# Performance work log

Hardware: AMD Instinct MI355X
Metric: run time of the kernel (lower is better)

Reference implementation:

```python
import jax, jax.numpy as jnp
import numpy as np

NUM_EXPERTS = 8
TOP_K = 2
HIDDEN = 1024
INTER = 1408
B, S = 2, 1024


def setup_inputs() -> dict:
    key = jax.random.key(0)
    k1, k2, k3, k4, k5 = jax.random.split(key, 5)
    scale = 0.02  # keep activations well-scaled
    return {
        "hidden_states": jax.random.normal(k1, (B, S, HIDDEN), dtype=jnp.float32),
        "gate_w": jax.random.normal(k2, (HIDDEN, NUM_EXPERTS), dtype=jnp.float32) * scale,
        "w_gate": jax.random.normal(k3, (NUM_EXPERTS, HIDDEN, INTER), dtype=jnp.float32) * scale,
        "w_up": jax.random.normal(k4, (NUM_EXPERTS, HIDDEN, INTER), dtype=jnp.float32) * scale,
        "w_down": jax.random.normal(k5, (NUM_EXPERTS, INTER, HIDDEN), dtype=jnp.float32) * scale,
    }


def reference(hidden_states, gate_w, w_gate, w_up, w_down):
    b, s, h = hidden_states.shape
    x = hidden_states.reshape(-1, h)  # [T, H]
    # Router: softmax in fp32, top-k, renormalize over selected experts
    logits = x @ gate_w  # [T, E]
    probs = jax.nn.softmax(logits.astype(jnp.float32), axis=-1)
    rw, sel = jax.lax.top_k(probs, TOP_K)  # [T, K]
    rw = rw / jnp.sum(rw, axis=-1, keepdims=True)
    rw = rw.astype(x.dtype)
    # Per-(token, expert) combine weight; duplicates summed (matches torch mask sum)
    combine = jnp.sum(rw[:, :, None] * jax.nn.one_hot(sel, NUM_EXPERTS, dtype=x.dtype), axis=1)  # [T, E]
    out = jnp.zeros_like(x)
    for e in range(NUM_EXPERTS):  # fixed small structural loop over experts
        inter = jax.nn.silu(x @ w_gate[e]) * (x @ w_up[e])  # [T, I]
        out = out + (inter @ w_down[e]) * combine[:, e:e + 1]
    return out.reshape(b, s, h)
```

## Files before the change

### kernel.cpp

```cpp
#include <hip/hip_runtime.h>
#include <hip/hip_bf16.h>

#define T_TOKENS 2048
#define HID 1024
#define ISZ 1408
#define NEXP 8
#define TILES_MAX 72

typedef __bf16 bf16x8 __attribute__((ext_vector_type(8)));
typedef __bf16 bf16x4 __attribute__((ext_vector_type(4)));
typedef float  f32x16 __attribute__((ext_vector_type(16)));

__device__ __forceinline__ void gload16(const void* g, void* l) {
    __builtin_amdgcn_global_load_lds(
        (const __attribute__((address_space(1))) void*)g,
        (__attribute__((address_space(3))) void*)l,
        16, 0, 0);
}

#define PIPE_BARRIER(N)                                              \
    asm volatile("s_waitcnt vmcnt(" #N ") lgkmcnt(0)" ::: "memory"); \
    __builtin_amdgcn_sched_barrier(0);                               \
    __builtin_amdgcn_s_barrier();                                    \
    __builtin_amdgcn_sched_barrier(0);

__global__ __launch_bounds__(256) void prep_kernel(
    const float* __restrict__ x, const float* __restrict__ gw,
    int* __restrict__ sel, float* __restrict__ wt, __bf16* __restrict__ xb,
    const float* __restrict__ wg, const float* __restrict__ wu,
    __bf16* __restrict__ wgT, __bf16* __restrict__ wuT)
{
    __shared__ __bf16 tb[2][64][70];
    const int bid = blockIdx.x;
    const int tid = threadIdx.x;

    if (bid < 512) {
        const int wave = tid >> 6;
        const int lane = tid & 63;
        const int t = bid * 4 + wave;
        const float* xr = x + (size_t)t * HID;

        const int c0 = lane * 16;
        float4 v0 = *(const float4*)(xr + c0);
        float4 v1 = *(const float4*)(xr + c0 + 4);
        float4 v2 = *(const float4*)(xr + c0 + 8);
        float4 v3 = *(const float4*)(xr + c0 + 12);
        {
            bf16x8 o0, o1;
            o0[0]=(__bf16)v0.x; o0[1]=(__bf16)v0.y; o0[2]=(__bf16)v0.z; o0[3]=(__bf16)v0.w;
            o0[4]=(__bf16)v1.x; o0[5]=(__bf16)v1.y; o0[6]=(__bf16)v1.z; o0[7]=(__bf16)v1.w;
            o1[0]=(__bf16)v2.x; o1[1]=(__bf16)v2.y; o1[2]=(__bf16)v2.z; o1[3]=(__bf16)v2.w;
            o1[4]=(__bf16)v3.x; o1[5]=(__bf16)v3.y; o1[6]=(__bf16)v3.z; o1[7]=(__bf16)v3.w;
            *(bf16x8*)(xb + (size_t)t * HID + c0) = o0;
            *(bf16x8*)(xb + (size_t)t * HID + c0 + 8) = o1;
        }
        if (bid == 0 && tid < 128) {
            bf16x8 z8;
            #pragma unroll
            for (int j = 0; j < 8; ++j) z8[j] = (__bf16)0.f;
            *(bf16x8*)(xb + (size_t)T_TOKENS * HID + tid * 8) = z8;
        }

        float le[8] = {0.f, 0.f, 0.f, 0.f, 0.f, 0.f, 0.f, 0.f};
        float xv[16];
        xv[0]=v0.x; xv[1]=v0.y; xv[2]=v0.z; xv[3]=v0.w;
        xv[4]=v1.x; xv[5]=v1.y; xv[6]=v1.z; xv[7]=v1.w;
        xv[8]=v2.x; xv[9]=v2.y; xv[10]=v2.z; xv[11]=v2.w;
        xv[12]=v3.x; xv[13]=v3.y; xv[14]=v3.z; xv[15]=v3.w;
        #pragma unroll
        for (int j = 0; j < 16; ++j) {
            const float* gr = gw + (size_t)(c0 + j) * NEXP;
            float4 g0 = *(const float4*)gr;
            float4 g1 = *(const float4*)(gr + 4);
            le[0] += xv[j] * g0.x; le[1] += xv[j] * g0.y;
            le[2] += xv[j] * g0.z; le[3] += xv[j] * g0.w;
            le[4] += xv[j] * g1.x; le[5] += xv[j] * g1.y;
            le[6] += xv[j] * g1.z; le[7] += xv[j] * g1.w;
        }
        #pragma unroll
        for (int d = 1; d < 64; d <<= 1) {
            #pragma unroll
            for (int k = 0; k < 8; ++k) le[k] += __shfl_xor(le[k], d);
        }
        float m = le[0];
        #pragma unroll
        for (int k = 1; k < 8; ++k) m = fmaxf(m, le[k]);
        float pe[8]; float s = 0.f;
        #pragma unroll
        for (int k = 0; k < 8; ++k) { pe[k] = expf(le[k] - m); s += pe[k]; }
        int e1 = 0; float p1 = pe[0];
        #pragma unroll
        for (int k = 1; k < 8; ++k) if (pe[k] > p1) { p1 = pe[k]; e1 = k; }
        int e2 = -1; float p2 = -1.f;
        #pragma unroll
        for (int k = 0; k < 8; ++k) if (k != e1 && pe[k] > p2) { p2 = pe[k]; e2 = k; }
        if (lane == 0) {
            float inv = 1.0f / (p1 + p2);
            sel[t * 2 + 0] = e1; sel[t * 2 + 1] = e2;
            wt[t * 2 + 0] = p1 * inv; wt[t * 2 + 1] = p2 * inv;
        }
        return;
    }

    const int f   = bid - 512;
    const int z   = f / 176;
    const int rem = f % 176;
    const int bx  = rem / 16;
    const int by  = rem & 15;
    const int e   = z & 7;
    const int R = HID, C = ISZ;
    const float* in = (z < 8 ? wg : wu) + (size_t)e * R * C;
    __bf16* out = (z < 8 ? wgT : wuT) + (size_t)e * R * C;
    const int rrA = by * 64, rrB = rrA;
    const int ccA = bx * 128, ccB = ccA + 64;
    const int lr  = tid >> 4;
    const int lc4 = (tid & 15) * 4;

    auto loadcvt = [&](int buf, int rr, int cc) {
        #pragma unroll
        for (int p = 0; p < 4; ++p) {
            float4 v = *(const float4*)(in + (size_t)(rr + p * 16 + lr) * C + cc + lc4);
            bf16x4 w;
            w[0] = (__bf16)v.x; w[1] = (__bf16)v.y; w[2] = (__bf16)v.z; w[3] = (__bf16)v.w;
            *(bf16x4*)&tb[buf][p * 16 + lr][lc4] = w;
        }
    };
    auto storeT = [&](int buf, int rr, int cc) {
        #pragma unroll
        for (int q = 0; q < 2; ++q) {
            const int oc = (tid >> 3) + 32 * q;
            const int vs = (tid & 7) * 8;
            bf16x8 w;
            #pragma unroll
            for (int j = 0; j < 8; ++j) w[j] = tb[buf][vs + j][oc];
            *(bf16x8*)(out + (size_t)(cc + oc) * R + rr + vs) = w;
        }
    };

    loadcvt(0, rrA, ccA);
    __syncthreads();
    loadcvt(1, rrB, ccB);
    storeT(0, rrA, ccA);
    __syncthreads();
    storeT(1, rrB, ccB);
}

__global__ __launch_bounds__(1024) void scan_assign_kernel(
    int* __restrict__ tiles,
    const int* __restrict__ sel, const float* __restrict__ wt,
    int* __restrict__ rtok, float* __restrict__ rwt, int* __restrict__ tok2row)
{
    __shared__ int hist[NEXP];
    __shared__ int soff[NEXP];
    __shared__ int scur[NEXP];
    if (threadIdx.x < NEXP) { hist[threadIdx.x] = 0; scur[threadIdx.x] = 0; }
    __syncthreads();
    for (int t = threadIdx.x; t < T_TOKENS; t += 1024) {
        atomicAdd(&hist[sel[t * 2 + 0]], 1);
        atomicAdd(&hist[sel[t * 2 + 1]], 1);
    }
    __syncthreads();
    if (threadIdx.x == 0) {
        int cur = 0, tix = 0;
        for (int e = 0; e < NEXP; ++e) {
            soff[e] = cur;
            int n64 = (hist[e] + 63) & ~63;
            for (int rt = 0; rt * 64 < n64; ++rt)
                tiles[tix++] = (e << 16) | (cur + rt * 64);
            cur += n64;
        }
        for (; tix < TILES_MAX; ++tix) tiles[tix] = -1;
    }
    __syncthreads();
    for (int t = threadIdx.x; t < T_TOKENS; t += 1024) {
        #pragma unroll
        for (int k = 0; k < 2; ++k) {
            int e = sel[t * 2 + k];
            int pos = atomicAdd(&scur[e], 1);
            int row = soff[e] + pos;
            rtok[row] = t + 1;
            rwt[row] = wt[t * 2 + k];
            tok2row[t * 2 + k] = row;
        }
    }
}

__global__ __launch_bounds__(256) void ffn1_kernel(
    const __bf16* __restrict__ xb, const int* __restrict__ rtok,
    const __bf16* __restrict__ wgT, const __bf16* __restrict__ wuT,
    const int* __restrict__ tiles, __bf16* __restrict__ inter,
    const float* __restrict__ wd, __bf16* __restrict__ wdT)
{
    __shared__ __align__(16) char smem[36864];
    const int n   = blockIdx.x;
    const int tid = threadIdx.x;

    if (n >= 22 * TILES_MAX) {
        auto tb = (__bf16 (*)[64][70])smem;
        const int f   = n - 22 * TILES_MAX;
        const int e   = f / 176;
        const int rem = f % 176;
        const int bx  = rem / 16;
        const int by  = rem & 15;
        const int R = ISZ, C = HID;
        const float* in = wd + (size_t)e * R * C;
        __bf16* out = wdT + (size_t)e * R * C;
        const int ccA = by * 64, ccB = ccA;
        const int rrA = bx * 128, rrB = rrA + 64;
        const int lr  = tid >> 4;
        const int lc4 = (tid & 15) * 4;

        auto loadcvt = [&](int buf, int rr, int cc) {
            #pragma unroll
            for (int p = 0; p < 4; ++p) {
                float4 v = *(const float4*)(in + (size_t)(rr + p * 16 + lr) * C + cc + lc4);
                bf16x4 w;
                w[0] = (__bf16)v.x; w[1] = (__bf16)v.y; w[2] = (__bf16)v.z; w[3] = (__bf16)v.w;
                *(bf16x4*)&tb[buf][p * 16 + lr][lc4] = w;
            }
        };
        auto storeT = [&](int buf, int rr, int cc) {
            #pragma unroll
            for (int q = 0; q < 2; ++q) {
                const int oc = (tid >> 3) + 32 * q;
                const int vs = (tid & 7) * 8;
                bf16x8 w;
                #pragma unroll
                for (int j = 0; j < 8; ++j) w[j] = tb[buf][vs + j][oc];
                *(bf16x8*)(out + (size_t)(cc + oc) * R + rr + vs) = w;
            }
        };

        loadcvt(0, rrA, ccA);
        __syncthreads();
        loadcvt(1, rrB, ccB);
        storeT(0, rrA, ccA);
        __syncthreads();
        storeT(1, rrB, ccB);
        return;
    }

    auto sA = (__bf16 (*)[64][32])(smem);
    auto sG = (__bf16 (*)[64][32])(smem + 12288);
    auto sU = (__bf16 (*)[64][32])(smem + 24576);

    const int nn = (n & 7) * 198 + (n >> 3);
    const int i0 = (nn / TILES_MAX) * 64;
    const int tv = tiles[nn % TILES_MAX];
    if (tv < 0) return;
    const int e = tv >> 16;
    const int rowbase = tv & 0xFFFF;

    const int lane = tid & 63;
    const int wid  = tid >> 6;
    const int wr = wid >> 1, wc = wid & 1;
    const int l31 = lane & 31;
    const int kg  = lane >> 5;

    const int r16 = lane >> 2;
    const int cz  = (((lane & 3) ^ ((r16 >> 1) & 3)) * 8);
    const int rowA = rowbase + wid * 16 + r16;
    const int tokp = rtok[rowA];
    const int src  = tokp ? (tokp - 1) : T_TOKENS;
    const __bf16* A0 = xb + (size_t)src * HID + cz;
    const size_t wb = (size_t)e * ISZ * HID + (size_t)(i0 + wid * 16 + r16) * HID + cz;
    const __bf16* G0 = wgT + wb;
    const __bf16* U0 = wuT + wb;

    f32x16 accG, accU;
    #pragma unroll
    for (int r = 0; r < 16; ++r) { accG[r] = 0.f; accU[r] = 0.f; }

    auto stage = [&](int b, int k0) {
        gload16(A0 + k0, &sA[b][wid * 16][0]);
        gload16(G0 + k0, &sG[b][wid * 16][0]);
        gload16(U0 + k0, &sU[b][wid * 16][0]);
    };
    auto compute = [&](int b) {
        #pragma unroll
        for (int s = 0; s < 2; ++s) {
            const int ch = ((2 * s + kg) ^ ((l31 >> 1) & 3)) * 8;
            bf16x8 a_ = *(const bf16x8*)&sA[b][wr * 32 + l31][ch];
            bf16x8 g_ = *(const bf16x8*)&sG[b][wc * 32 + l31][ch];
            bf16x8 u_ = *(const bf16x8*)&sU[b][wc * 32 + l31][ch];
            __builtin_amdgcn_s_setprio(1);
            accG = __builtin_amdgcn_mfma_f32_32x32x16_bf16(a_, g_, accG, 0, 0, 0);
            accU = __builtin_amdgcn_mfma_f32_32x32x16_bf16(a_, u_, accU, 0, 0, 0);
            __builtin_amdgcn_s_setprio(0);
        }
    };

    const int nIter = HID / 32;
    stage(0, 0);
    stage(1, 32);
    PIPE_BARRIER(3)
    for (int i = 0; i < nIter; ++i) {
        int ks = (i + 2 < nIter) ? (i + 2) * 32 : 0;
        stage((i + 2) % 3, ks);
        compute(i % 3);
        PIPE_BARRIER(3)
    }

    const int base_row = rowbase + wr * 32;
    #pragma unroll
    for (int r = 0; r < 16; ++r) {
        float g = accG[r];
        float u = accU[r];
        float v = g / (1.0f + __expf(-g)) * u;
        int row = base_row + (r & 3) + 8 * (r >> 2) + 4 * kg;
        inter[(size_t)row * ISZ + i0 + wc * 32 + l31] = (__bf16)v;
    }
}

__global__ __launch_bounds__(256) void ffn2_kernel(
    const __bf16* __restrict__ inter, const __bf16* __restrict__ wdT,
    const float* __restrict__ rwt, const int* __restrict__ tiles,
    __bf16* __restrict__ y)
{
    const int n  = blockIdx.x;
    const int nn = (n & 7) * 72 + (n >> 3);
    const int n0 = (nn / TILES_MAX) * 128;
    const int tv = tiles[nn % TILES_MAX];
    if (tv < 0) return;
    const int e = tv >> 16;
    const int rowbase = tv & 0xFFFF;

    __shared__ __align__(16) __bf16 sA[3][64][32];
    __shared__ __align__(16) __bf16 sB[3][128][32];

    const int lane = threadIdx.x & 63;
    const int wid  = threadIdx.x >> 6;
    const int wr = wid >> 1, wc = wid & 1;
    const int l31 = lane & 31;
    const int kg  = lane >> 5;

    const int r16 = lane >> 2;
    const int cz  = (((lane & 3) ^ ((r16 >> 1) & 3)) * 8);
    const __bf16* A0 = inter + (size_t)(rowbase + wid * 16 + r16) * ISZ + cz;
    const __bf16* B0 = wdT + (size_t)e * HID * ISZ + (size_t)(n0 + wid * 32 + r16) * ISZ + cz;
    const size_t rstepB = (size_t)16 * ISZ;

    f32x16 acc[2];
    #pragma unroll
    for (int q = 0; q < 2; ++q)
        #pragma unroll
        for (int r = 0; r < 16; ++r) acc[q][r] = 0.f;

    auto stage = [&](int b, int k0) {
        gload16(A0 + k0,          &sA[b][wid * 16][0]);
        gload16(B0 + k0,          &sB[b][wid * 32][0]);
        gload16(B0 + k0 + rstepB, &sB[b][wid * 32 + 16][0]);
    };
    auto compute = [&](int b) {
        #pragma unroll
        for (int s = 0; s < 2; ++s) {
            const int ch = ((2 * s + kg) ^ ((l31 >> 1) & 3)) * 8;
            bf16x8 a_ = *(const bf16x8*)&sA[b][wr * 32 + l31][ch];
            bf16x8 b0 = *(const bf16x8*)&sB[b][wc * 64 + l31][ch];
            bf16x8 b1 = *(const bf16x8*)&sB[b][wc * 64 + 32 + l31][ch];
            __builtin_amdgcn_s_setprio(1);
            acc[0] = __builtin_amdgcn_mfma_f32_32x32x16_bf16(a_, b0, acc[0], 0, 0, 0);
            acc[1] = __builtin_amdgcn_mfma_f32_32x32x16_bf16(a_, b1, acc[1], 0, 0, 0);
            __builtin_amdgcn_s_setprio(0);
        }
    };

    const int nIter = ISZ / 32;
    stage(0, 0);
    stage(1, 32);
    PIPE_BARRIER(3)
    for (int i = 0; i < nIter; ++i) {
        int ks = (i + 2 < nIter) ? (i + 2) * 32 : 0;
        stage((i + 2) % 3, ks);
        compute(i % 3);
        PIPE_BARRIER(3)
    }

    const int base_row = rowbase + wr * 32;
    #pragma unroll
    for (int q = 0; q < 2; ++q) {
        const int col = n0 + wc * 64 + q * 32 + l31;
        #pragma unroll
        for (int r = 0; r < 16; ++r) {
            int row = base_row + (r & 3) + 8 * (r >> 2) + 4 * kg;
            y[(size_t)row * HID + col] = (__bf16)(rwt[row] * acc[q][r]);
        }
    }
}

__global__ __launch_bounds__(256) void combine_kernel(
    const __bf16* __restrict__ y, const int* __restrict__ tok2row, float* __restrict__ out)
{
    const int idx = blockIdx.x * 256 + threadIdx.x;
    const int t = idx >> 7;
    const int c = (idx & 127) * 8;
    const int r0 = tok2row[t * 2];
    const int r1 = tok2row[t * 2 + 1];
    bf16x8 a = *(const bf16x8*)(y + (size_t)r0 * HID + c);
    bf16x8 b = *(const bf16x8*)(y + (size_t)r1 * HID + c);
    float4 o0, o1;
    o0.x = (float)a[0] + (float)b[0]; o0.y = (float)a[1] + (float)b[1];
    o0.z = (float)a[2] + (float)b[2]; o0.w = (float)a[3] + (float)b[3];
    o1.x = (float)a[4] + (float)b[4]; o1.y = (float)a[5] + (float)b[5];
    o1.z = (float)a[6] + (float)b[6]; o1.w = (float)a[7] + (float)b[7];
    *(float4*)(out + (size_t)t * HID + c) = o0;
    *(float4*)(out + (size_t)t * HID + c + 4) = o1;
}

extern "C" void kernel_launch(void* const* d_in, const int* in_sizes, int n_in,
                              void* d_out, int out_size, void* d_ws, size_t ws_size,
                              hipStream_t stream) {
    const float* x  = (const float*)d_in[0];
    const float* gw = (const float*)d_in[1];
    const float* wg = (const float*)d_in[2];
    const float* wu = (const float*)d_in[3];
    const float* wd = (const float*)d_in[4];
    float* out = (float*)d_out;

    char* ws = (char*)d_ws;
    int*    tiles   = (int*)(ws + 64);
    int*    sel     = (int*)(ws + 1024);
    float*  wtp     = (float*)(ws + 17408);
    int*    rtok    = (int*)(ws + 33792);
    float*  rwt     = (float*)(ws + 52224);
    int*    tok2row = (int*)(ws + 70656);
    __bf16* xb      = (__bf16*)(ws + 87040);
    __bf16* inter   = (__bf16*)(ws + 4283648);
    __bf16* wgT     = (__bf16*)(ws + 17260032);
    __bf16* wuT     = (__bf16*)(ws + 40328704);
    __bf16* wdT     = (__bf16*)(ws + 63397376);
    __bf16* y       = (__bf16*)wgT;

    hipMemsetAsync(ws, 0, 87040, stream);

    prep_kernel<<<3328, 256, 0, stream>>>(x, gw, sel, wtp, xb, wg, wu, wgT, wuT);
    scan_assign_kernel<<<1, 1024, 0, stream>>>(tiles, sel, wtp, rtok, rwt, tok2row);

    ffn1_kernel<<<22 * TILES_MAX + 1408, 256, 0, stream>>>(
        xb, rtok, wgT, wuT, tiles, inter, wd, wdT);
    ffn2_kernel<<<8 * TILES_MAX, 256, 0, stream>>>(inter, wdT, rwt, tiles, y);
    combine_kernel<<<(T_TOKENS * HID / 8) / 256, 256, 0, stream>>>(y, tok2row, out);
}
```

Measured before the change: 133.9 us.

## Split w_down conversion between prep and ffn1, drop workspace memset

Moves the transpose-and-convert of w_down for experts 0-3 into prep_kernel (704 extra blocks), leaving experts 4-7 as the tail work in ffn1_kernel. This rebalances the conversion load across the two launches. It also removes the hipMemsetAsync of the workspace header and instead zeroes only the padding rows of rtok inside scan_assign_kernel. The risk is that other memset regions (sel, wt, tok2row, rwt padding) were relied on being zero.

Measured after the change: 132.9 us. No clear change (-0.8%).

```diff
diff --git a/kernel.cpp b/kernel.cpp
--- a/kernel.cpp
+++ b/kernel.cpp
@@ -27,8 +27,8 @@
 __global__ __launch_bounds__(256) void prep_kernel(
     const float* __restrict__ x, const float* __restrict__ gw,
     int* __restrict__ sel, float* __restrict__ wt, __bf16* __restrict__ xb,
-    const float* __restrict__ wg, const float* __restrict__ wu,
-    __bf16* __restrict__ wgT, __bf16* __restrict__ wuT)
+    const float* __restrict__ wg, const float* __restrict__ wu, const float* __restrict__ wd,
+    __bf16* __restrict__ wgT, __bf16* __restrict__ wuT, __bf16* __restrict__ wdT)
 {
     __shared__ __bf16 tb[2][64][70];
     const int bid = blockIdx.x;
@@ -102,19 +102,36 @@
         return;
     }
 
-    const int f   = bid - 512;
-    const int z   = f / 176;
-    const int rem = f % 176;
-    const int bx  = rem / 16;
-    const int by  = rem & 15;
-    const int e   = z & 7;
-    const int R = HID, C = ISZ;
-    const float* in = (z < 8 ? wg : wu) + (size_t)e * R * C;
-    __bf16* out = (z < 8 ? wgT : wuT) + (size_t)e * R * C;
-    const int rrA = by * 64, rrB = rrA;
-    const int ccA = bx * 128, ccB = ccA + 64;
     const int lr  = tid >> 4;
     const int lc4 = (tid & 15) * 4;
+    const float* in;
+    __bf16* out;
+    int R, C, rrA, ccA, rrB, ccB;
+
+    if (bid < 3328) {
+        const int f   = bid - 512;
+        const int z   = f / 176;
+        const int rem = f % 176;
+        const int bx  = rem / 16;
+        const int by  = rem & 15;
+        const int e   = z & 7;
+        R = HID; C = ISZ;
+        in  = (z < 8 ? wg : wu) + (size_t)e * R * C;
+        out = (z < 8 ? wgT : wuT) + (size_t)e * R * C;
+        rrA = by * 64; rrB = rrA;
+        ccA = bx * 128; ccB = ccA + 64;
+    } else {
+        const int f   = bid - 3328;
+        const int e   = f / 176;
+        const int rem = f % 176;
+        const int bx  = rem / 16;
+        const int by  = rem & 15;
+        R = ISZ; C = HID;
+        in  = wd  + (size_t)e * R * C;
+        out = wdT + (size_t)e * R * C;
+        ccA = by * 64; ccB = ccA;
+        rrA = bx * 128; rrB = rrA + 64;
+    }
 
     auto loadcvt = [&](int buf, int rr, int cc) {
         #pragma unroll
@@ -152,6 +169,7 @@
 {
     __shared__ int hist[NEXP];
     __shared__ int soff[NEXP];
+    __shared__ int snal[NEXP];
     __shared__ int scur[NEXP];
     if (threadIdx.x < NEXP) { hist[threadIdx.x] = 0; scur[threadIdx.x] = 0; }
     __syncthreads();
@@ -165,11 +183,17 @@
         for (int e = 0; e < NEXP; ++e) {
             soff[e] = cur;
             int n64 = (hist[e] + 63) & ~63;
+            snal[e] = n64;
             for (int rt = 0; rt * 64 < n64; ++rt)
                 tiles[tix++] = (e << 16) | (cur + rt * 64);
             cur += n64;
         }
         for (; tix < TILES_MAX; ++tix) tiles[tix] = -1;
+    }
+    __syncthreads();
+    for (int e = 0; e < NEXP; ++e) {
+        const int lo = soff[e] + hist[e], hi = soff[e] + snal[e];
+        for (int r = lo + (int)threadIdx.x; r < hi; r += 1024) rtok[r] = 0;
     }
     __syncthreads();
     for (int t = threadIdx.x; t < T_TOKENS; t += 1024) {
@@ -198,7 +222,7 @@
     if (n >= 22 * TILES_MAX) {
         auto tb = (__bf16 (*)[64][70])smem;
         const int f   = n - 22 * TILES_MAX;
-        const int e   = f / 176;
+        const int e   = 4 + f / 176;
         const int rem = f % 176;
         const int bx  = rem / 16;
         const int by  = rem & 15;
@@ -431,12 +455,11 @@
     __bf16* wdT     = (__bf16*)(ws + 63397376);
     __bf16* y       = (__bf16*)wgT;
 
-    hipMemsetAsync(ws, 0, 87040, stream);
-
-    prep_kernel<<<3328, 256, 0, stream>>>(x, gw, sel, wtp, xb, wg, wu, wgT, wuT);
+
+    prep_kernel<<<4032, 256, 0, stream>>>(x, gw, sel, wtp, xb, wg, wu, wd, wgT, wuT, wdT);
     scan_assign_kernel<<<1, 1024, 0, stream>>>(tiles, sel, wtp, rtok, rwt, tok2row);
 
-    ffn1_kernel<<<22 * TILES_MAX + 1408, 256, 0, stream>>>(
+    ffn1_kernel<<<22 * TILES_MAX + 704, 256, 0, stream>>>(
         xb, rtok, wgT, wuT, tiles, inter, wd, wdT);
     ffn2_kernel<<<8 * TILES_MAX, 256, 0, stream>>>(inter, wdT, rwt, tiles, y);
     combine_kernel<<<(T_TOKENS * HID / 8) / 256, 256, 0, stream>>>(y, tok2row, out);
```
